# Kernel tuning notes

Measured on AMD Instinct MI355X. Metric: run time of the kernel, lower is better.

The kernel has to match this reference:

```python
import jax, jax.numpy as jnp
import numpy as np

N = 6144
ATT_DIM = 128
HID = int(ATT_DIM * 0.75)  # 96
EDGE_EMB_DIM = 20
N_EDGE_TYPES = 3
E_PER_TYPE = 100000
NUM_LAYERS = 2
NUM_HEADS = 2
NEG_SLOPE = 0.2


def _leaky(x):
    return jnp.where(x > 0, x, NEG_SLOPE * x)


def setup_inputs() -> dict:
    key = jax.random.key(0)
    ks = jax.random.split(key, 8)
    inputs = jax.random.normal(ks[0], (N, ATT_DIM), dtype=jnp.float32)
    edges = jax.random.randint(ks[1], (N_EDGE_TYPES, 2, E_PER_TYPE), 0, N, dtype=jnp.int64)
    # ScoringNetwork params (Linear stored as [in, out])
    W1 = jax.random.normal(ks[2], (ATT_DIM, HID), dtype=jnp.float32) * (1.0 / np.sqrt(ATT_DIM))
    b1 = jnp.zeros((HID,), dtype=jnp.float32)
    W2 = jax.random.normal(ks[3], (HID, 1), dtype=jnp.float32) * (1.0 / np.sqrt(HID))
    b2 = jnp.zeros((1,), dtype=jnp.float32)
    # shared edge-type embeddings
    edge_emb = jax.random.normal(ks[4], (N_EDGE_TYPES, EDGE_EMB_DIM), dtype=jnp.float32) * 0.1
    # per-layer, per-head attention weights [L, H, edge_emb_dim+2, 1]
    attn_w = jax.random.normal(ks[5], (NUM_LAYERS, NUM_HEADS, EDGE_EMB_DIM + 2, 1), dtype=jnp.float32) * 0.1
    return {"inputs": inputs, "edges": edges, "W1": W1, "b1": b1,
            "W2": W2, "b2": b2, "edge_emb": edge_emb, "attn_w": attn_w}


def reference(inputs, edges, W1, b1, W2, b2, edge_emb, attn_w):
    n = inputs.shape[0]
    T, _, E = edges.shape
    src = edges[:, 0, :].reshape(-1)  # [T*E]
    tgt = edges[:, 1, :].reshape(-1)  # [T*E]
    # ScoringNetwork: linear2(leakyrelu(linear1(x)))  -> [N, 1]
    scores = _leaky(inputs @ W1 + b1) @ W2 + b2
    L, H = attn_w.shape[0], attn_w.shape[1]
    for l in range(L):
        acc = jnp.zeros_like(scores)
        s = scores[:, 0]  # [N]
        for h in range(H):
            w = attn_w[l, h, :, 0]  # [edge_emb_dim + 2]
            # concat([src_score, edge_emb, tgt_score]) @ w, computed factored
            emb_score = edge_emb @ w[1:-1]  # [T]
            e = w[0] * s[src] + jnp.repeat(emb_score, E) + w[-1] * s[tgt]  # [T*E]
            # scatter-add into dense NxN (accumulates across edge types)
            A = jnp.zeros((n, n), dtype=scores.dtype).at[src, tgt].add(e)
            att = jax.nn.softmax(_leaky(A), axis=-1)  # dense row softmax (incl. non-edges)
            acc = acc + att @ scores
        scores = acc / H
    return scores
```

## Files before the change

### kernel.cpp

```cpp
#include <hip/hip_runtime.h>

#define N_NODES 6144
#define ATTD 128
#define HIDD 96
#define EPT 100000
#define NTYPE 3
#define NEDGE (NTYPE * EPT)
#define BCAP 128
#define CPAD 16
#define PSTRIDE 16
#define NCELL 64
#define NEG 0.2f
#define BUCKET_BLOCKS ((NEDGE + 255) / 256)
#define MLP_BLOCKS (N_NODES / 2)

__global__ void k_init(const float* __restrict__ attn_w,
                       const float* __restrict__ edge_emb,
                       float* __restrict__ params, int* __restrict__ rcnt,
                       float* __restrict__ part0, float* __restrict__ part1) {
    int i = blockIdx.x * blockDim.x + threadIdx.x;
    if (i < N_NODES * CPAD) rcnt[i] = 0;
    if (i < NCELL * PSTRIDE) { part0[i] = 0.f; part1[i] = 0.f; }
    if (i < 4) {
        const float* w = attn_w + i * 22;
        float* p = params + i * 8;
        p[0] = w[0];
        p[1] = w[21];
        for (int ty = 0; ty < NTYPE; ++ty) {
            float acc = 0.f;
            for (int j = 0; j < 20; ++j) acc += edge_emb[ty * 20 + j] * w[1 + j];
            p[2 + ty] = acc;
        }
    }
}

__global__ void k_build(const int* __restrict__ edges, int* __restrict__ rcnt,
                        int* __restrict__ bucket,
                        const float* __restrict__ X, const float* __restrict__ W1,
                        const float* __restrict__ b1, const float* __restrict__ W2,
                        const float* __restrict__ b2, float* __restrict__ s,
                        float* __restrict__ part0) {
    int bid = blockIdx.x;
    if (bid < BUCKET_BLOCKS) {
        int k = bid * 256 + threadIdx.x;
        if (k < NEDGE) {
            int t = k / EPT;
            int e = k - t * EPT;
            int src = edges[t * (2 * EPT) + e];
            int tgt = edges[t * (2 * EPT) + EPT + e];
            int pos = atomicAdd(&rcnt[src * CPAD], 1);
            if (pos < BCAP) bucket[src * BCAP + pos] = (t << 13) | tgt;
        }
        return;
    }
    int half = threadIdx.x >> 7;
    int tid  = threadIdx.x & 127;
    int row  = (bid - BUCKET_BLOCKS) * 2 + half;
    __shared__ float xs[2][ATTD];
    __shared__ float red[2][2];
    __shared__ float sred[2];
    xs[half][tid] = X[row * ATTD + tid];
    __syncthreads();
    float val = 0.f;
    if (tid < HIDD) {
        float acc = b1[tid];
#pragma unroll
        for (int k = 0; k < ATTD; ++k) acc += xs[half][k] * W1[k * HIDD + tid];
        float h = acc > 0.f ? acc : NEG * acc;
        val = h * W2[tid];
    }
#pragma unroll
    for (int off = 32; off; off >>= 1) val += __shfl_down(val, off, 64);
    if ((threadIdx.x & 63) == 0) red[half][tid >> 6] = val;
    __syncthreads();
    if (tid == 0) {
        float r = red[half][0] + red[half][1] + b2[0];
        s[row] = r;
        sred[half] = r;
    }
    __syncthreads();
    if (threadIdx.x == 0)
        atomicAdd(&part0[((bid - BUCKET_BLOCKS) & (NCELL - 1)) * PSTRIDE],
                  sred[0] + sred[1]);
}

__global__ void k_gather1(const int* __restrict__ rcnt, int* bucket,
                          const float* __restrict__ s, const float* __restrict__ params,
                          const float* __restrict__ part0, float* __restrict__ s2,
                          int* __restrict__ cw2, int* __restrict__ cnt2,
                          float* __restrict__ part1) {
    int lane = threadIdx.x & 63;
    int wv   = threadIdx.x >> 6;
    int u    = blockIdx.x * 4 + wv;
    __shared__ int hk[4 * 256];
    __shared__ int hc[4 * 256];
    __shared__ float stot_s;
    __shared__ float wsum[4];
    int* K = hk + wv * 256;
    int* C = hc + wv * 256;
#pragma unroll
    for (int j = lane; j < 256; j += 64) { K[j] = -1; C[j] = 0; }
    if (wv == 0) {
        float v = part0[lane * PSTRIDE];
#pragma unroll
        for (int off = 32; off; off >>= 1) v += __shfl_down(v, off, 64);
        if (lane == 0) stot_s = v;
    }
    __syncthreads();
    int d = rcnt[u * CPAD];
    if (d > BCAP) d = BCAP;
    for (int i = lane; i < d; i += 64) {
        int raw = bucket[u * BCAP + i];
        int v = raw & 8191;
        int t = raw >> 13;
        unsigned slot = ((unsigned)v * 2654435761u) >> 24;
        while (true) {
            int prev = atomicCAS(&K[slot], -1, v);
            if (prev == -1 || prev == v) break;
            slot = (slot + 1) & 255;
        }
        atomicAdd(&C[slot], 1 << (10 * t));
    }
    __syncthreads();
    const float* p0 = params + 0;
    const float* p1 = params + 8;
    float su = s[u];
    float w00 = p0[0], w01 = p0[1], e00 = p0[2], e01 = p0[3], e02 = p0[4];
    float w10 = p1[0], w11 = p1[1], e10 = p1[2], e11 = p1[3], e12 = p1[4];
    float num0 = 0.f, den0 = 0.f, num1 = 0.f, den1 = 0.f;
    int base = 0;
#pragma unroll
    for (int it = 0; it < 4; ++it) {
        int j = it * 64 + lane;
        int key = K[j];
        bool live = key >= 0;
        unsigned long long m = __ballot(live);
        if (live) {
            int cw = C[j];
            int idx = base + __popcll(m & ((1ull << lane) - 1ull));
            bucket[u * BCAP + idx] = key;
            cw2[u * BCAP + idx] = cw;
            float c0 = (float)(cw & 1023);
            float c1 = (float)((cw >> 10) & 1023);
            float c2 = (float)((cw >> 20) & 1023);
            float Cc = c0 + c1 + c2;
            float sv = s[key];
            float A0 = Cc * (w00 * su + w01 * sv) + c0 * e00 + c1 * e01 + c2 * e02;
            float la0 = A0 > 0.f ? A0 : NEG * A0;
            float g0 = expf(la0) - 1.f;
            num0 += g0 * sv; den0 += g0;
            float A1 = Cc * (w10 * su + w11 * sv) + c0 * e10 + c1 * e11 + c2 * e12;
            float la1 = A1 > 0.f ? A1 : NEG * A1;
            float g1 = expf(la1) - 1.f;
            num1 += g1 * sv; den1 += g1;
        }
        base += __popcll(m);
    }
#pragma unroll
    for (int off = 32; off; off >>= 1) {
        num0 += __shfl_down(num0, off, 64);
        den0 += __shfl_down(den0, off, 64);
        num1 += __shfl_down(num1, off, 64);
        den1 += __shfl_down(den1, off, 64);
    }
    if (lane == 0) {
        cnt2[u] = base;
        float S = stot_s;
        float r0 = (S + num0) / ((float)N_NODES + den0);
        float r1 = (S + num1) / ((float)N_NODES + den1);
        float val = 0.5f * (r0 + r1);
        s2[u] = val;
        wsum[wv] = val;
    }
    __syncthreads();
    if (threadIdx.x == 0)
        atomicAdd(&part1[(blockIdx.x & (NCELL - 1)) * PSTRIDE],
                  wsum[0] + wsum[1] + wsum[2] + wsum[3]);
}

__global__ void k_gather2(const int* __restrict__ cnt2, const int* __restrict__ bucket,
                          const int* __restrict__ cw2, const float* __restrict__ s,
                          const float* __restrict__ params, const float* __restrict__ part1,
                          float* __restrict__ dst) {
    int lane = threadIdx.x & 63;
    int wv   = threadIdx.x >> 6;
    int u    = blockIdx.x * 4 + wv;
    __shared__ float stot_s;
    if (wv == 0) {
        float v = part1[lane * PSTRIDE];
#pragma unroll
        for (int off = 32; off; off >>= 1) v += __shfl_down(v, off, 64);
        if (lane == 0) stot_s = v;
    }
    __syncthreads();
    float su = s[u];
    const float* p0 = params + 16;
    const float* p1 = params + 24;
    float w00 = p0[0], w01 = p0[1], e00 = p0[2], e01 = p0[3], e02 = p0[4];
    float w10 = p1[0], w11 = p1[1], e10 = p1[2], e11 = p1[3], e12 = p1[4];
    float num0 = 0.f, den0 = 0.f, num1 = 0.f, den1 = 0.f;
    int d = cnt2[u];
    for (int i = lane; i < d; i += 64) {
        int v  = bucket[u * BCAP + i];
        int cw = cw2[u * BCAP + i];
        float c0 = (float)(cw & 1023);
        float c1 = (float)((cw >> 10) & 1023);
        float c2 = (float)((cw >> 20) & 1023);
        float Cc = c0 + c1 + c2;
        float sv = s[v];
        float A0 = Cc * (w00 * su + w01 * sv) + c0 * e00 + c1 * e01 + c2 * e02;
        float la0 = A0 > 0.f ? A0 : NEG * A0;
        float g0 = expf(la0) - 1.f;
        num0 += g0 * sv; den0 += g0;
        float A1 = Cc * (w10 * su + w11 * sv) + c0 * e10 + c1 * e11 + c2 * e12;
        float la1 = A1 > 0.f ? A1 : NEG * A1;
        float g1 = expf(la1) - 1.f;
        num1 += g1 * sv; den1 += g1;
    }
#pragma unroll
    for (int off = 32; off; off >>= 1) {
        num0 += __shfl_down(num0, off, 64);
        den0 += __shfl_down(den0, off, 64);
        num1 += __shfl_down(num1, off, 64);
        den1 += __shfl_down(den1, off, 64);
    }
    if (lane == 0) {
        float S = stot_s;
        float r0 = (S + num0) / ((float)N_NODES + den0);
        float r1 = (S + num1) / ((float)N_NODES + den1);
        dst[u] = 0.5f * (r0 + r1);
    }
}

extern "C" void kernel_launch(void* const* d_in, const int* in_sizes, int n_in,
                              void* d_out, int out_size, void* d_ws, size_t ws_size,
                              hipStream_t stream) {
    const float* X        = (const float*)d_in[0];
    const int*   edges    = (const int*)d_in[1];
    const float* W1       = (const float*)d_in[2];
    const float* b1       = (const float*)d_in[3];
    const float* W2       = (const float*)d_in[4];
    const float* b2       = (const float*)d_in[5];
    const float* edge_emb = (const float*)d_in[6];
    const float* attn_w   = (const float*)d_in[7];
    float* out = (float*)d_out;

    char* w = (char*)d_ws;
    float* params = (float*)w; w += 256;
    float* part0  = (float*)w; w += NCELL * PSTRIDE * sizeof(float);
    float* part1  = (float*)w; w += NCELL * PSTRIDE * sizeof(float);
    float* s      = (float*)w; w += N_NODES * sizeof(float);
    float* s2     = (float*)w; w += N_NODES * sizeof(float);
    int*   cnt2   = (int*)w;   w += N_NODES * sizeof(int);
    int*   rcnt   = (int*)w;   w += N_NODES * CPAD * sizeof(int);
    int*   bucket = (int*)w;   w += N_NODES * BCAP * sizeof(int);
    int*   cw2    = (int*)w;   w += N_NODES * BCAP * sizeof(int);

    k_init<<<(N_NODES * CPAD) / 256, 256, 0, stream>>>(attn_w, edge_emb, params,
                                                       rcnt, part0, part1);
    k_build<<<BUCKET_BLOCKS + MLP_BLOCKS, 256, 0, stream>>>(edges, rcnt, bucket,
                                                            X, W1, b1, W2, b2, s, part0);
    k_gather1<<<N_NODES / 4, 256, 0, stream>>>(rcnt, bucket, s, params, part0,
                                               s2, cw2, cnt2, part1);
    k_gather2<<<N_NODES / 4, 256, 0, stream>>>(cnt2, bucket, cw2, s2, params, part1,
                                               out);
}
```

Before: 50.36 us.

## Split per-row edge counters into sub-buckets and drop the init kernel

Each source row's atomic counter is split into four padded sub-counters chosen by edge index, which spreads contention in the bucketing atomics. The separate init kernel is replaced by a hipMemsetAsync over a contiguous zero region. The attention parameters are now recomputed per block in shared memory. The merged neighbor list is written as interleaved int2 pairs instead of two arrays. This adds a memset launch and per-block parameter recomputation, and caps each sub-bucket at 48 entries, which could drop edges for rows whose edges land unevenly across sub-buckets.

```diff
diff --git a/kernel.cpp b/kernel.cpp
--- a/kernel.cpp
+++ b/kernel.cpp
@@ -6,33 +6,16 @@
 #define EPT 100000
 #define NTYPE 3
 #define NEDGE (NTYPE * EPT)
-#define BCAP 128
-#define CPAD 16
+#define SUBS 4
+#define SUBCAP 48
+#define RSTRIDE (SUBS * SUBCAP)
+#define CSTRIDE 16
+#define MCAP 128
 #define PSTRIDE 16
 #define NCELL 64
 #define NEG 0.2f
 #define BUCKET_BLOCKS ((NEDGE + 255) / 256)
 #define MLP_BLOCKS (N_NODES / 2)
-
-__global__ void k_init(const float* __restrict__ attn_w,
-                       const float* __restrict__ edge_emb,
-                       float* __restrict__ params, int* __restrict__ rcnt,
-                       float* __restrict__ part0, float* __restrict__ part1) {
-    int i = blockIdx.x * blockDim.x + threadIdx.x;
-    if (i < N_NODES * CPAD) rcnt[i] = 0;
-    if (i < NCELL * PSTRIDE) { part0[i] = 0.f; part1[i] = 0.f; }
-    if (i < 4) {
-        const float* w = attn_w + i * 22;
-        float* p = params + i * 8;
-        p[0] = w[0];
-        p[1] = w[21];
-        for (int ty = 0; ty < NTYPE; ++ty) {
-            float acc = 0.f;
-            for (int j = 0; j < 20; ++j) acc += edge_emb[ty * 20 + j] * w[1 + j];
-            p[2 + ty] = acc;
-        }
-    }
-}
 
 __global__ void k_build(const int* __restrict__ edges, int* __restrict__ rcnt,
                         int* __restrict__ bucket,
@@ -48,14 +31,16 @@
             int e = k - t * EPT;
             int src = edges[t * (2 * EPT) + e];
             int tgt = edges[t * (2 * EPT) + EPT + e];
-            int pos = atomicAdd(&rcnt[src * CPAD], 1);
-            if (pos < BCAP) bucket[src * BCAP + pos] = (t << 13) | tgt;
+            int sub = k & (SUBS - 1);
+            int pos = atomicAdd(&rcnt[(src * SUBS + sub) * CSTRIDE], 1);
+            if (pos < SUBCAP) bucket[src * RSTRIDE + sub * SUBCAP + pos] = (t << 13) | tgt;
         }
         return;
     }
     int half = threadIdx.x >> 7;
     int tid  = threadIdx.x & 127;
-    int row  = (bid - BUCKET_BLOCKS) * 2 + half;
+    int mbid = bid - BUCKET_BLOCKS;
+    int row  = mbid * 2 + half;
     __shared__ float xs[2][ATTD];
     __shared__ float red[2][2];
     __shared__ float sred[2];
@@ -64,7 +49,7 @@
     float val = 0.f;
     if (tid < HIDD) {
         float acc = b1[tid];
-#pragma unroll
+#pragma unroll 8
         for (int k = 0; k < ATTD; ++k) acc += xs[half][k] * W1[k * HIDD + tid];
         float h = acc > 0.f ? acc : NEG * acc;
         val = h * W2[tid];
@@ -80,22 +65,33 @@
     }
     __syncthreads();
     if (threadIdx.x == 0)
-        atomicAdd(&part0[((bid - BUCKET_BLOCKS) & (NCELL - 1)) * PSTRIDE],
-                  sred[0] + sred[1]);
-}
-
-__global__ void k_gather1(const int* __restrict__ rcnt, int* bucket,
-                          const float* __restrict__ s, const float* __restrict__ params,
+        atomicAdd(&part0[(mbid & (NCELL - 1)) * PSTRIDE], sred[0] + sred[1]);
+}
+
+__global__ void k_gather1(const int* __restrict__ rcnt, const int* __restrict__ bucket,
+                          const float* __restrict__ s,
+                          const float* __restrict__ edge_emb,
+                          const float* __restrict__ attn_w,
                           const float* __restrict__ part0, float* __restrict__ s2,
-                          int* __restrict__ cw2, int* __restrict__ cnt2,
+                          int2* __restrict__ mlist, int* __restrict__ cnt2,
                           float* __restrict__ part1) {
-    int lane = threadIdx.x & 63;
-    int wv   = threadIdx.x >> 6;
-    int u    = blockIdx.x * 4 + wv;
+    int tid = threadIdx.x, lane = tid & 63, wv = tid >> 6, bid = blockIdx.x;
     __shared__ int hk[4 * 256];
     __shared__ int hc[4 * 256];
+    __shared__ float pl[32];
     __shared__ float stot_s;
     __shared__ float wsum[4];
+    if (tid < 4) {
+        const float* w = attn_w + tid * 22;
+        float* p = pl + tid * 8;
+        p[0] = w[0];
+        p[1] = w[21];
+        for (int ty = 0; ty < NTYPE; ++ty) {
+            float acc = 0.f;
+            for (int j = 0; j < 20; ++j) acc += edge_emb[ty * 20 + j] * w[1 + j];
+            p[2 + ty] = acc;
+        }
+    }
     int* K = hk + wv * 256;
     int* C = hc + wv * 256;
 #pragma unroll
@@ -107,26 +103,27 @@
         if (lane == 0) stot_s = v;
     }
     __syncthreads();
-    int d = rcnt[u * CPAD];
-    if (d > BCAP) d = BCAP;
-    for (int i = lane; i < d; i += 64) {
-        int raw = bucket[u * BCAP + i];
-        int v = raw & 8191;
-        int t = raw >> 13;
-        unsigned slot = ((unsigned)v * 2654435761u) >> 24;
-        while (true) {
-            int prev = atomicCAS(&K[slot], -1, v);
-            if (prev == -1 || prev == v) break;
-            slot = (slot + 1) & 255;
-        }
-        atomicAdd(&C[slot], 1 << (10 * t));
-    }
-    __syncthreads();
-    const float* p0 = params + 0;
-    const float* p1 = params + 8;
+    const int u = bid * 4 + wv;
+    for (int sdx = 0; sdx < SUBS; ++sdx) {
+        int d = rcnt[(u * SUBS + sdx) * CSTRIDE];
+        if (d > SUBCAP) d = SUBCAP;
+        for (int i = lane; i < d; i += 64) {
+            int raw = bucket[u * RSTRIDE + sdx * SUBCAP + i];
+            int v = raw & 8191;
+            int t = raw >> 13;
+            unsigned slot = ((unsigned)v * 2654435761u) >> 24;
+            while (true) {
+                int prev = atomicCAS(&K[slot], -1, v);
+                if (prev == -1 || prev == v) break;
+                slot = (slot + 1) & 255;
+            }
+            atomicAdd(&C[slot], 1 << (10 * t));
+        }
+    }
+    __syncthreads();
     float su = s[u];
-    float w00 = p0[0], w01 = p0[1], e00 = p0[2], e01 = p0[3], e02 = p0[4];
-    float w10 = p1[0], w11 = p1[1], e10 = p1[2], e11 = p1[3], e12 = p1[4];
+    float w00 = pl[0], w01 = pl[1], e00 = pl[2], e01 = pl[3], e02 = pl[4];
+    float w10 = pl[8], w11 = pl[9], e10 = pl[10], e11 = pl[11], e12 = pl[12];
     float num0 = 0.f, den0 = 0.f, num1 = 0.f, den1 = 0.f;
     int base = 0;
 #pragma unroll
@@ -138,8 +135,7 @@
         if (live) {
             int cw = C[j];
             int idx = base + __popcll(m & ((1ull << lane) - 1ull));
-            bucket[u * BCAP + idx] = key;
-            cw2[u * BCAP + idx] = cw;
+            mlist[u * MCAP + idx] = make_int2(key, cw);
             float c0 = (float)(cw & 1023);
             float c1 = (float)((cw >> 10) & 1023);
             float c2 = (float)((cw >> 20) & 1023);
@@ -173,19 +169,30 @@
         wsum[wv] = val;
     }
     __syncthreads();
-    if (threadIdx.x == 0)
-        atomicAdd(&part1[(blockIdx.x & (NCELL - 1)) * PSTRIDE],
+    if (tid == 0)
+        atomicAdd(&part1[(bid & (NCELL - 1)) * PSTRIDE],
                   wsum[0] + wsum[1] + wsum[2] + wsum[3]);
 }
 
-__global__ void k_gather2(const int* __restrict__ cnt2, const int* __restrict__ bucket,
-                          const int* __restrict__ cw2, const float* __restrict__ s,
-                          const float* __restrict__ params, const float* __restrict__ part1,
-                          float* __restrict__ dst) {
-    int lane = threadIdx.x & 63;
-    int wv   = threadIdx.x >> 6;
-    int u    = blockIdx.x * 4 + wv;
+__global__ void k_gather2(const int* __restrict__ cnt2, const int2* __restrict__ mlist,
+                          const float* __restrict__ s,
+                          const float* __restrict__ edge_emb,
+                          const float* __restrict__ attn_w,
+                          const float* __restrict__ part1, float* __restrict__ dst) {
+    int tid = threadIdx.x, lane = tid & 63, wv = tid >> 6, bid = blockIdx.x;
+    __shared__ float pl[32];
     __shared__ float stot_s;
+    if (tid < 4) {
+        const float* w = attn_w + tid * 22;
+        float* p = pl + tid * 8;
+        p[0] = w[0];
+        p[1] = w[21];
+        for (int ty = 0; ty < NTYPE; ++ty) {
+            float acc = 0.f;
+            for (int j = 0; j < 20; ++j) acc += edge_emb[ty * 20 + j] * w[1 + j];
+            p[2 + ty] = acc;
+        }
+    }
     if (wv == 0) {
         float v = part1[lane * PSTRIDE];
 #pragma unroll
@@ -193,16 +200,16 @@
         if (lane == 0) stot_s = v;
     }
     __syncthreads();
+    const int u = bid * 4 + wv;
     float su = s[u];
-    const float* p0 = params + 16;
-    const float* p1 = params + 24;
-    float w00 = p0[0], w01 = p0[1], e00 = p0[2], e01 = p0[3], e02 = p0[4];
-    float w10 = p1[0], w11 = p1[1], e10 = p1[2], e11 = p1[3], e12 = p1[4];
+    float w00 = pl[16], w01 = pl[17], e00 = pl[18], e01 = pl[19], e02 = pl[20];
+    float w10 = pl[24], w11 = pl[25], e10 = pl[26], e11 = pl[27], e12 = pl[28];
     float num0 = 0.f, den0 = 0.f, num1 = 0.f, den1 = 0.f;
     int d = cnt2[u];
     for (int i = lane; i < d; i += 64) {
-        int v  = bucket[u * BCAP + i];
-        int cw = cw2[u * BCAP + i];
+        int2 vc = mlist[u * MCAP + i];
+        int v  = vc.x;
+        int cw = vc.y;
         float c0 = (float)(cw & 1023);
         float c1 = (float)((cw >> 10) & 1023);
         float c2 = (float)((cw >> 20) & 1023);
@@ -246,22 +253,21 @@
     float* out = (float*)d_out;
 
     char* w = (char*)d_ws;
-    float* params = (float*)w; w += 256;
     float* part0  = (float*)w; w += NCELL * PSTRIDE * sizeof(float);
     float* part1  = (float*)w; w += NCELL * PSTRIDE * sizeof(float);
+    int*   rcnt   = (int*)w;   w += N_NODES * SUBS * CSTRIDE * sizeof(int);
+    size_t zbytes = (size_t)(w - (char*)d_ws);
     float* s      = (float*)w; w += N_NODES * sizeof(float);
     float* s2     = (float*)w; w += N_NODES * sizeof(float);
     int*   cnt2   = (int*)w;   w += N_NODES * sizeof(int);
-    int*   rcnt   = (int*)w;   w += N_NODES * CPAD * sizeof(int);
-    int*   bucket = (int*)w;   w += N_NODES * BCAP * sizeof(int);
-    int*   cw2    = (int*)w;   w += N_NODES * BCAP * sizeof(int);
-
-    k_init<<<(N_NODES * CPAD) / 256, 256, 0, stream>>>(attn_w, edge_emb, params,
-                                                       rcnt, part0, part1);
+    int*   bucket = (int*)w;   w += N_NODES * RSTRIDE * sizeof(int);
+    int2*  mlist  = (int2*)w;
+
+    hipMemsetAsync(d_ws, 0, zbytes, stream);
     k_build<<<BUCKET_BLOCKS + MLP_BLOCKS, 256, 0, stream>>>(edges, rcnt, bucket,
                                                             X, W1, b1, W2, b2, s, part0);
-    k_gather1<<<N_NODES / 4, 256, 0, stream>>>(rcnt, bucket, s, params, part0,
-                                               s2, cw2, cnt2, part1);
-    k_gather2<<<N_NODES / 4, 256, 0, stream>>>(cnt2, bucket, cw2, s2, params, part1,
-                                               out);
-}
+    k_gather1<<<N_NODES / 4, 256, 0, stream>>>(rcnt, bucket, s, edge_emb, attn_w,
+                                               part0, s2, mlist, cnt2, part1);
+    k_gather2<<<N_NODES / 4, 256, 0, stream>>>(cnt2, mlist, s2, edge_emb, attn_w,
+                                               part1, out);
+}
```

New measurement: 54.48 us. +8.2%, slower.
